# Kernel optimization log

Hardware: AMD Instinct MI355X
Metric: run time of the kernel (lower is better)

Reference implementation:

```python
import jax, jax.numpy as jnp
import numpy as np

N = 100000   # nodes
E = 1600000  # edges (avg degree 16)
DIN, DH, DOUT = 128, 64, 40


def setup_inputs() -> dict:
    key = jax.random.key(0)
    ks = jax.random.split(key, 6)
    x = jax.random.normal(ks[0], (N, DIN), dtype=jnp.float32)
    edge_index = jax.random.randint(ks[1], (2, E), 0, N, dtype=jnp.int32)
    s1 = float(1.0 / np.sqrt(DIN))
    s2 = float(1.0 / np.sqrt(DH))
    W1 = jax.random.uniform(ks[2], (DIN, DH), jnp.float32, -s1, s1)
    b1 = jax.random.uniform(ks[3], (DH,), jnp.float32, -s1, s1)
    W2 = jax.random.uniform(ks[4], (DH, DOUT), jnp.float32, -s2, s2)
    b2 = jax.random.uniform(ks[5], (DOUT,), jnp.float32, -s2, s2)
    return {"x": x, "W1": W1, "b1": b1, "W2": W2, "b2": b2, "edge_index": edge_index}


def _gcn_conv(x, W, b, src, dst):
    """PyG GCNConv: add self-loops, symmetric degree normalization, scatter-add."""
    n = x.shape[0]
    h = x @ W  # [N, F_out] — transform before propagation (PyG order)
    ones = jnp.ones(src.shape[0], dtype=h.dtype)
    deg = jax.ops.segment_sum(ones, dst, num_segments=n) + 1.0  # +1 for self-loop
    dinv = jax.lax.rsqrt(deg)  # deg >= 1, no zero guard needed
    norm = dinv[src] * dinv[dst]  # [E]
    agg = jax.ops.segment_sum(h[src] * norm[:, None], dst, num_segments=n)
    agg = agg + h * (dinv * dinv)[:, None]  # self-loop messages
    return agg + b


def reference(x, W1, b1, W2, b2, edge_index):
    src, dst = edge_index[0], edge_index[1]
    h = jax.nn.relu(_gcn_conv(x, W1, b1, src, dst))
    out = _gcn_conv(h, W2, b2, src, dst)
    return jax.nn.log_softmax(out, axis=1)
```

## Files before the change

### kernel.cpp

```cpp
#include <hip/hip_runtime.h>
#include <math.h>

#define N_NODES 100000
#define N_EDGES 1600000
#define DIN 128
#define DH 64
#define DOUT 40

#define NB 256
#define BN 391
#define CAP 8192
#define BIN_BLOCKS 512
#define EPB 3125

typedef unsigned short u16;
typedef unsigned int u32;

__device__ inline float bf2f(u16 u) {
    return __uint_as_float(((u32)u) << 16);
}
__device__ inline u16 f2bf(float f) {
    u32 u = __float_as_uint(f);
    u32 r = (u + 0x7FFFu + ((u >> 16) & 1u)) >> 16;
    return (u16)r;
}
__device__ inline void acc4(uint2 v, float& a0, float& a1, float& a2, float& a3) {
    a0 += __uint_as_float(v.x << 16);
    a1 += __uint_as_float(v.x & 0xffff0000u);
    a2 += __uint_as_float(v.y << 16);
    a3 += __uint_as_float(v.y & 0xffff0000u);
}


__global__ __launch_bounds__(256) void k_bin(const int* __restrict__ src,
                                             const int* __restrict__ dst,
                                             int* __restrict__ gcur,
                                             u32* __restrict__ staged) {
    __shared__ int hist[NB];
    __shared__ int base[NB];
    __shared__ int cur[NB];
    int t = threadIdx.x;
    for (int i = t; i < NB; i += 256) { hist[i] = 0; cur[i] = 0; }
    __syncthreads();
    int e0 = blockIdx.x * EPB;
    int e1 = e0 + EPB; if (e1 > N_EDGES) e1 = N_EDGES;
    for (int e = e0 + t; e < e1; e += 256)
        atomicAdd(&hist[dst[e] / BN], 1);
    __syncthreads();
    for (int i = t; i < NB; i += 256) {
        int h = hist[i];
        base[i] = h ? atomicAdd(&gcur[i], h) : 0;
    }
    __syncthreads();
    for (int e = e0 + t; e < e1; e += 256) {
        int d = dst[e], s = src[e];
        int b = d / BN;
        int dl = d - b * BN;
        int r = base[b] + atomicAdd(&cur[b], 1);
        if (r < CAP) staged[(size_t)b * CAP + r] = (u32)s | ((u32)dl << 17);
    }
}


__global__ __launch_bounds__(256) void k_csr(const int* __restrict__ gcur,
                                             const u32* __restrict__ staged,
                                             int* __restrict__ csr,
                                             int4* __restrict__ meta,
                                             float* __restrict__ dinv) {
    __shared__ u32 sedge[CAP];
    __shared__ int lcsr[CAP];
    __shared__ int hist[BN];
    __shared__ int lrs[BN];
    __shared__ int cur[BN];
    __shared__ int sbuf[256];
    int b = blockIdx.x, t = threadIdx.x;

    int part = 0;
    for (int i = t; i < b; i += 256) {
        int c = gcur[i]; if (c > CAP) c = CAP;
        part += c;
    }
    sbuf[t] = part;
    __syncthreads();
    for (int off = 128; off; off >>= 1) {
        if (t < off) sbuf[t] += sbuf[t + off];
        __syncthreads();
    }
    int base_ = sbuf[0];
    __syncthreads();

    int cnt = gcur[b]; if (cnt > CAP) cnt = CAP;
    for (int i = t; i < BN; i += 256) hist[i] = 0;
    for (int i = t; i < cnt; i += 256) sedge[i] = staged[(size_t)b * CAP + i];
    __syncthreads();
    for (int i = t; i < cnt; i += 256) atomicAdd(&hist[sedge[i] >> 17], 1);
    __syncthreads();

    int v0 = (2 * t < BN) ? hist[2 * t] : 0;
    int v1 = (2 * t + 1 < BN) ? hist[2 * t + 1] : 0;
    int s = v0 + v1;
    sbuf[t] = s;
    __syncthreads();
    for (int off = 1; off < 256; off <<= 1) {
        int add = (t >= off) ? sbuf[t - off] : 0;
        __syncthreads();
        sbuf[t] += add;
        __syncthreads();
    }
    int excl = sbuf[t] - s;
    if (2 * t < BN)     { lrs[2 * t] = excl;      cur[2 * t] = excl; }
    if (2 * t + 1 < BN) { lrs[2 * t + 1] = excl + v0; cur[2 * t + 1] = excl + v0; }
    __syncthreads();

    for (int i = t; i < cnt; i += 256) {
        u32 p = sedge[i];
        int pos = atomicAdd(&cur[p >> 17], 1);
        lcsr[pos] = (int)(p & 0x1FFFF);
    }
    __syncthreads();

    for (int i = t; i < cnt; i += 256) csr[base_ + i] = lcsr[i];
    int n0 = b * BN;
    for (int i = t; i < BN; i += 256) {
        int n = n0 + i;
        if (n < N_NODES) {
            int dg = hist[i];
            float dv = rsqrtf((float)dg + 1.0f);
            meta[n] = make_int4(base_ + lrs[i], dg, __float_as_int(dv), 0);
            dinv[n] = dv;
        }
    }
}


__global__ __launch_bounds__(256) void k_gemm1(const float* __restrict__ x,
                                               const float* __restrict__ W1,
                                               const float* __restrict__ dinv,
                                               u16* __restrict__ h1s) {
    __shared__ float xs[64 * 132];
    __shared__ float wsh[DIN * DH];
    int t = threadIdx.x;
    int row0 = blockIdx.x * 64;

    for (int it = 0; it < 8; ++it) {
        int idx = (it * 256 + t) * 4;
        int r = idx >> 7, c = idx & 127;
        float4 v = make_float4(0.f, 0.f, 0.f, 0.f);
        if (row0 + r < N_NODES) v = *(const float4*)&x[(size_t)(row0 + r) * DIN + c];
        *(float4*)&xs[r * 132 + c] = v;
    }
    for (int it = 0; it < 8; ++it) {
        int idx = (it * 256 + t) * 4;
        *(float4*)&wsh[idx] = *(const float4*)&W1[idx];
    }
    __syncthreads();

    int tr = t & 15;
    int tc = t >> 4;
    float acc[4][4] = {};
    for (int k = 0; k < DIN; ++k) {
        float4 wv = *(const float4*)&wsh[k * DH + tr * 4];
#pragma unroll
        for (int i = 0; i < 4; ++i) {
            float xv = xs[(tc * 4 + i) * 132 + k];
            acc[i][0] += xv * wv.x;
            acc[i][1] += xv * wv.y;
            acc[i][2] += xv * wv.z;
            acc[i][3] += xv * wv.w;
        }
    }
#pragma unroll
    for (int i = 0; i < 4; ++i) {
        int row = row0 + tc * 4 + i;
        if (row < N_NODES) {
            float dv = dinv[row];
            ushort4 o;
            o.x = f2bf(acc[i][0] * dv);
            o.y = f2bf(acc[i][1] * dv);
            o.z = f2bf(acc[i][2] * dv);
            o.w = f2bf(acc[i][3] * dv);
            *(ushort4*)&h1s[(size_t)row * DH + tr * 4] = o;
        }
    }
}


__global__ __launch_bounds__(256) void k_agg1(const u16* __restrict__ h1s,
                                              const int4* __restrict__ meta,
                                              const int* __restrict__ csr,
                                              const float* __restrict__ b1,
                                              float* __restrict__ h1) {
    int node = blockIdx.x * 4 + (threadIdx.x >> 6);
    if (node >= N_NODES) return;
    node = __builtin_amdgcn_readfirstlane(node);
    int lane = threadIdx.x & 63;
    int es = lane >> 4, fp = lane & 15;
    int4 me = meta[node];
    int s0 = me.x, d = me.y;
    float dv = __int_as_float(me.z);
    const uint2* rows = (const uint2*)h1s;
    float a0 = 0.f, a1 = 0.f, a2 = 0.f, a3 = 0.f;
    if (es == 0) acc4(rows[(u32)(node * 16 + fp)], a0, a1, a2, a3);
    for (int base = 0; base < d; base += 64) {
        int nn = d - base; if (nn > 64) nn = 64;
        int myidx = (lane < nn) ? csr[s0 + base + lane] : 0;
        int j = 0;
        for (; j + 16 <= nn; j += 16) {
            int x0 = __builtin_amdgcn_ds_bpermute((j + es) * 4, myidx);
            int x1 = __builtin_amdgcn_ds_bpermute((j + 4 + es) * 4, myidx);
            int x2 = __builtin_amdgcn_ds_bpermute((j + 8 + es) * 4, myidx);
            int x3 = __builtin_amdgcn_ds_bpermute((j + 12 + es) * 4, myidx);
            uint2 v0 = rows[(u32)(x0 * 16 + fp)];
            uint2 v1 = rows[(u32)(x1 * 16 + fp)];
            uint2 v2 = rows[(u32)(x2 * 16 + fp)];
            uint2 v3 = rows[(u32)(x3 * 16 + fp)];
            acc4(v0, a0, a1, a2, a3);
            acc4(v1, a0, a1, a2, a3);
            acc4(v2, a0, a1, a2, a3);
            acc4(v3, a0, a1, a2, a3);
        }
        for (; j < nn; j += 4) {
            int x = __builtin_amdgcn_ds_bpermute((j + es) * 4, myidx);
            if (j + es < nn) acc4(rows[(u32)(x * 16 + fp)], a0, a1, a2, a3);
        }
    }
    a0 += __shfl_xor(a0, 16, 64); a1 += __shfl_xor(a1, 16, 64);
    a2 += __shfl_xor(a2, 16, 64); a3 += __shfl_xor(a3, 16, 64);
    a0 += __shfl_xor(a0, 32, 64); a1 += __shfl_xor(a1, 32, 64);
    a2 += __shfl_xor(a2, 32, 64); a3 += __shfl_xor(a3, 32, 64);
    if (es == 0) {
        float4 bv = ((const float4*)b1)[fp];
        float4 o;
        o.x = fmaxf(a0 * dv + bv.x, 0.f);
        o.y = fmaxf(a1 * dv + bv.y, 0.f);
        o.z = fmaxf(a2 * dv + bv.z, 0.f);
        o.w = fmaxf(a3 * dv + bv.w, 0.f);
        ((float4*)h1)[(u32)(node * 16 + fp)] = o;
    }
}


__global__ __launch_bounds__(256) void k_gemm2(const float* __restrict__ h1,
                                               const float* __restrict__ W2,
                                               const float* __restrict__ dinv,
                                               u16* __restrict__ h2s) {
    __shared__ float xs[64 * 68];
    __shared__ float wsh[DH * DOUT];
    int t = threadIdx.x;
    int row0 = blockIdx.x * 64;

    for (int it = 0; it < 4; ++it) {
        int idx = (it * 256 + t) * 4;
        int r = idx >> 6, c = idx & 63;
        float4 v = make_float4(0.f, 0.f, 0.f, 0.f);
        if (row0 + r < N_NODES) v = *(const float4*)&h1[(size_t)(row0 + r) * DH + c];
        *(float4*)&xs[r * 68 + c] = v;
    }
    for (int idx = t * 4; idx < DH * DOUT; idx += 1024) {
        *(float4*)&wsh[idx] = *(const float4*)&W2[idx];
    }
    __syncthreads();

    int fg = t & 7;
    int rg = t >> 3;
    float acc[2][5] = {};
    for (int k = 0; k < DH; ++k) {
        float x0 = xs[(rg * 2 + 0) * 68 + k];
        float x1 = xs[(rg * 2 + 1) * 68 + k];
#pragma unroll
        for (int j = 0; j < 5; ++j) {
            float w = wsh[k * DOUT + fg * 5 + j];
            acc[0][j] += x0 * w;
            acc[1][j] += x1 * w;
        }
    }
#pragma unroll
    for (int i = 0; i < 2; ++i) {
        int row = row0 + rg * 2 + i;
        if (row < N_NODES) {
            float dvv = dinv[row];
#pragma unroll
            for (int j = 0; j < 5; ++j)
                h2s[(size_t)row * 64 + fg * 5 + j] = f2bf(acc[i][j] * dvv);
        }
    }
}


__global__ __launch_bounds__(256) void k_agg2(const u16* __restrict__ h2s,
                                              const int4* __restrict__ meta,
                                              const int* __restrict__ csr,
                                              const float* __restrict__ b2,
                                              float* __restrict__ out) {
    int node = blockIdx.x * 4 + (threadIdx.x >> 6);
    if (node >= N_NODES) return;
    node = __builtin_amdgcn_readfirstlane(node);
    int lane = threadIdx.x & 63;
    int es = lane >> 4, fp = lane & 15;
    bool act = fp < 10;
    int4 me = meta[node];
    int s0 = me.x, d = me.y;
    float dv = __int_as_float(me.z);
    const uint2* rows = (const uint2*)h2s;
    float a0 = 0.f, a1 = 0.f, a2 = 0.f, a3 = 0.f;
    if (es == 0 && act) acc4(rows[(u32)(node * 16 + fp)], a0, a1, a2, a3);
    for (int base = 0; base < d; base += 64) {
        int nn = d - base; if (nn > 64) nn = 64;
        int myidx = (lane < nn) ? csr[s0 + base + lane] : 0;
        int j = 0;
        for (; j + 16 <= nn; j += 16) {
            int x0 = __builtin_amdgcn_ds_bpermute((j + es) * 4, myidx);
            int x1 = __builtin_amdgcn_ds_bpermute((j + 4 + es) * 4, myidx);
            int x2 = __builtin_amdgcn_ds_bpermute((j + 8 + es) * 4, myidx);
            int x3 = __builtin_amdgcn_ds_bpermute((j + 12 + es) * 4, myidx);
            if (act) {
                uint2 v0 = rows[(u32)(x0 * 16 + fp)];
                uint2 v1 = rows[(u32)(x1 * 16 + fp)];
                uint2 v2 = rows[(u32)(x2 * 16 + fp)];
                uint2 v3 = rows[(u32)(x3 * 16 + fp)];
                acc4(v0, a0, a1, a2, a3);
                acc4(v1, a0, a1, a2, a3);
                acc4(v2, a0, a1, a2, a3);
                acc4(v3, a0, a1, a2, a3);
            }
        }
        for (; j < nn; j += 4) {
            int x = __builtin_amdgcn_ds_bpermute((j + es) * 4, myidx);
            if (act && j + es < nn) acc4(rows[(u32)(x * 16 + fp)], a0, a1, a2, a3);
        }
    }
    a0 += __shfl_xor(a0, 16, 64); a1 += __shfl_xor(a1, 16, 64);
    a2 += __shfl_xor(a2, 16, 64); a3 += __shfl_xor(a3, 16, 64);
    a0 += __shfl_xor(a0, 32, 64); a1 += __shfl_xor(a1, 32, 64);
    a2 += __shfl_xor(a2, 32, 64); a3 += __shfl_xor(a3, 32, 64);

    float4 bv = act ? ((const float4*)b2)[fp] : make_float4(0.f, 0.f, 0.f, 0.f);
    float v0 = act ? a0 * dv + bv.x : -INFINITY;
    float v1 = act ? a1 * dv + bv.y : -INFINITY;
    float v2 = act ? a2 * dv + bv.z : -INFINITY;
    float v3 = act ? a3 * dv + bv.w : -INFINITY;
    float m = fmaxf(fmaxf(v0, v1), fmaxf(v2, v3));
    m = fmaxf(m, __shfl_xor(m, 1, 64));
    m = fmaxf(m, __shfl_xor(m, 2, 64));
    m = fmaxf(m, __shfl_xor(m, 4, 64));
    m = fmaxf(m, __shfl_xor(m, 8, 64));
    float ex = act ? (expf(v0 - m) + expf(v1 - m) + expf(v2 - m) + expf(v3 - m)) : 0.f;
    ex += __shfl_xor(ex, 1, 64);
    ex += __shfl_xor(ex, 2, 64);
    ex += __shfl_xor(ex, 4, 64);
    ex += __shfl_xor(ex, 8, 64);
    float lse = m + logf(ex);
    if (es == 0 && act) {
        float4 o = make_float4(v0 - lse, v1 - lse, v2 - lse, v3 - lse);
        *(float4*)&out[(u32)(node * 40 + fp * 4)] = o;
    }
}


extern "C" void kernel_launch(void* const* d_in, const int* in_sizes, int n_in,
                              void* d_out, int out_size, void* d_ws, size_t ws_size,
                              hipStream_t stream) {
    const float* x  = (const float*)d_in[0];
    const float* W1 = (const float*)d_in[1];
    const float* b1 = (const float*)d_in[2];
    const float* W2 = (const float*)d_in[3];
    const float* b2 = (const float*)d_in[4];
    const int* eidx = (const int*)d_in[5];
    const int* srcp = eidx;
    const int* dstp = eidx + N_EDGES;
    float* out = (float*)d_out;

    char* w = (char*)d_ws;
    int* gcur    = (int*)w;   w += sizeof(int) * NB;
    float* dinv  = (float*)w; w += sizeof(float) * N_NODES + 48;
    int4* meta   = (int4*)w;  w += sizeof(int4) * N_NODES;
    u32* staged  = (u32*)w;   w += sizeof(u32) * (size_t)NB * CAP;
    int* csr     = (int*)w;   w += sizeof(int) * N_EDGES;
    u16* h1s     = (u16*)w;   w += sizeof(u16) * (size_t)N_NODES * DH;
    float* h1    = (float*)w; w += sizeof(float) * (size_t)N_NODES * DH;
    u16* h2s     = h1s;

    hipMemsetAsync(gcur, 0, sizeof(int) * NB, stream);
    k_bin<<<BIN_BLOCKS, 256, 0, stream>>>(srcp, dstp, gcur, staged);
    k_csr<<<NB, 256, 0, stream>>>(gcur, staged, csr, meta, dinv);
    k_gemm1<<<(N_NODES + 63) / 64, 256, 0, stream>>>(x, W1, dinv, h1s);
    k_agg1<<<(N_NODES + 3) / 4, 256, 0, stream>>>(h1s, meta, csr, b1, h1);
    k_gemm2<<<(N_NODES + 63) / 64, 256, 0, stream>>>(h1, W2, dinv, h2s);
    k_agg2<<<(N_NODES + 3) / 4, 256, 0, stream>>>(h2s, meta, csr, b2, out);
}
```

Baseline: 222.0 us.

## Store features as fp16 and accumulate aggregation with packed half2 adds

Intermediate node features move from bf16 storage with fp32 accumulation to fp16 storage with packed half2 accumulation in both aggregation kernels, cross-lane reductions included. This cuts the unpack and add instruction count per gathered row by doing two features per packed add. The first GEMM also reads four k values per LDS load, with a new row padding. The trade is lower accumulation precision and a risk of fp16 overflow or rounding error on high-degree nodes, while gather memory traffic stays the same.

```diff
diff --git a/kernel.cpp b/kernel.cpp
--- a/kernel.cpp
+++ b/kernel.cpp
@@ -1,4 +1,5 @@
 #include <hip/hip_runtime.h>
+#include <hip/hip_fp16.h>
 #include <math.h>
 
 #define N_NODES 100000
@@ -16,19 +17,11 @@
 typedef unsigned short u16;
 typedef unsigned int u32;
 
-__device__ inline float bf2f(u16 u) {
-    return __uint_as_float(((u32)u) << 16);
-}
-__device__ inline u16 f2bf(float f) {
-    u32 u = __float_as_uint(f);
-    u32 r = (u + 0x7FFFu + ((u >> 16) & 1u)) >> 16;
-    return (u16)r;
-}
-__device__ inline void acc4(uint2 v, float& a0, float& a1, float& a2, float& a3) {
-    a0 += __uint_as_float(v.x << 16);
-    a1 += __uint_as_float(v.x & 0xffff0000u);
-    a2 += __uint_as_float(v.y << 16);
-    a3 += __uint_as_float(v.y & 0xffff0000u);
+__device__ inline __half2 u2h(u32 u) {
+    union { u32 x; __half2 h; } c; c.x = u; return c.h;
+}
+__device__ inline u32 h2u(__half2 h) {
+    union { __half2 h; u32 x; } c; c.h = h; return c.x;
 }
 
 
@@ -137,7 +130,7 @@
                                                const float* __restrict__ W1,
                                                const float* __restrict__ dinv,
                                                u16* __restrict__ h1s) {
-    __shared__ float xs[64 * 132];
+    __shared__ float xs[64 * 140];
     __shared__ float wsh[DIN * DH];
     int t = threadIdx.x;
     int row0 = blockIdx.x * 64;
@@ -147,7 +140,7 @@
         int r = idx >> 7, c = idx & 127;
         float4 v = make_float4(0.f, 0.f, 0.f, 0.f);
         if (row0 + r < N_NODES) v = *(const float4*)&x[(size_t)(row0 + r) * DIN + c];
-        *(float4*)&xs[r * 132 + c] = v;
+        *(float4*)&xs[r * 140 + c] = v;
     }
     for (int it = 0; it < 8; ++it) {
         int idx = (it * 256 + t) * 4;
@@ -158,15 +151,22 @@
     int tr = t & 15;
     int tc = t >> 4;
     float acc[4][4] = {};
-    for (int k = 0; k < DIN; ++k) {
-        float4 wv = *(const float4*)&wsh[k * DH + tr * 4];
+    for (int kb = 0; kb < DIN; kb += 4) {
+        float4 w0 = *(const float4*)&wsh[(kb + 0) * DH + tr * 4];
+        float4 w1 = *(const float4*)&wsh[(kb + 1) * DH + tr * 4];
+        float4 w2 = *(const float4*)&wsh[(kb + 2) * DH + tr * 4];
+        float4 w3 = *(const float4*)&wsh[(kb + 3) * DH + tr * 4];
 #pragma unroll
         for (int i = 0; i < 4; ++i) {
-            float xv = xs[(tc * 4 + i) * 132 + k];
-            acc[i][0] += xv * wv.x;
-            acc[i][1] += xv * wv.y;
-            acc[i][2] += xv * wv.z;
-            acc[i][3] += xv * wv.w;
+            float4 xv = *(const float4*)&xs[(tc * 4 + i) * 140 + kb];
+            acc[i][0] += xv.x * w0.x; acc[i][1] += xv.x * w0.y;
+            acc[i][2] += xv.x * w0.z; acc[i][3] += xv.x * w0.w;
+            acc[i][0] += xv.y * w1.x; acc[i][1] += xv.y * w1.y;
+            acc[i][2] += xv.y * w1.z; acc[i][3] += xv.y * w1.w;
+            acc[i][0] += xv.z * w2.x; acc[i][1] += xv.z * w2.y;
+            acc[i][2] += xv.z * w2.z; acc[i][3] += xv.z * w2.w;
+            acc[i][0] += xv.w * w3.x; acc[i][1] += xv.w * w3.y;
+            acc[i][2] += xv.w * w3.z; acc[i][3] += xv.w * w3.w;
         }
     }
 #pragma unroll
@@ -175,10 +175,10 @@
         if (row < N_NODES) {
             float dv = dinv[row];
             ushort4 o;
-            o.x = f2bf(acc[i][0] * dv);
-            o.y = f2bf(acc[i][1] * dv);
-            o.z = f2bf(acc[i][2] * dv);
-            o.w = f2bf(acc[i][3] * dv);
+            o.x = __half_as_ushort(__float2half(acc[i][0] * dv));
+            o.y = __half_as_ushort(__float2half(acc[i][1] * dv));
+            o.z = __half_as_ushort(__float2half(acc[i][2] * dv));
+            o.w = __half_as_ushort(__float2half(acc[i][3] * dv));
             *(ushort4*)&h1s[(size_t)row * DH + tr * 4] = o;
         }
     }
@@ -199,8 +199,11 @@
     int s0 = me.x, d = me.y;
     float dv = __int_as_float(me.z);
     const uint2* rows = (const uint2*)h1s;
-    float a0 = 0.f, a1 = 0.f, a2 = 0.f, a3 = 0.f;
-    if (es == 0) acc4(rows[(u32)(node * 16 + fp)], a0, a1, a2, a3);
+    __half2 A01 = __float2half2_rn(0.f), A23 = __float2half2_rn(0.f);
+    if (es == 0) {
+        uint2 v = rows[(u32)(node * 16 + fp)];
+        A01 = u2h(v.x); A23 = u2h(v.y);
+    }
     for (int base = 0; base < d; base += 64) {
         int nn = d - base; if (nn > 64) nn = 64;
         int myidx = (lane < nn) ? csr[s0 + base + lane] : 0;
@@ -214,27 +217,30 @@
             uint2 v1 = rows[(u32)(x1 * 16 + fp)];
             uint2 v2 = rows[(u32)(x2 * 16 + fp)];
             uint2 v3 = rows[(u32)(x3 * 16 + fp)];
-            acc4(v0, a0, a1, a2, a3);
-            acc4(v1, a0, a1, a2, a3);
-            acc4(v2, a0, a1, a2, a3);
-            acc4(v3, a0, a1, a2, a3);
+            A01 = __hadd2(A01, u2h(v0.x)); A23 = __hadd2(A23, u2h(v0.y));
+            A01 = __hadd2(A01, u2h(v1.x)); A23 = __hadd2(A23, u2h(v1.y));
+            A01 = __hadd2(A01, u2h(v2.x)); A23 = __hadd2(A23, u2h(v2.y));
+            A01 = __hadd2(A01, u2h(v3.x)); A23 = __hadd2(A23, u2h(v3.y));
         }
         for (; j < nn; j += 4) {
             int x = __builtin_amdgcn_ds_bpermute((j + es) * 4, myidx);
-            if (j + es < nn) acc4(rows[(u32)(x * 16 + fp)], a0, a1, a2, a3);
-        }
-    }
-    a0 += __shfl_xor(a0, 16, 64); a1 += __shfl_xor(a1, 16, 64);
-    a2 += __shfl_xor(a2, 16, 64); a3 += __shfl_xor(a3, 16, 64);
-    a0 += __shfl_xor(a0, 32, 64); a1 += __shfl_xor(a1, 32, 64);
-    a2 += __shfl_xor(a2, 32, 64); a3 += __shfl_xor(a3, 32, 64);
+            if (j + es < nn) {
+                uint2 v = rows[(u32)(x * 16 + fp)];
+                A01 = __hadd2(A01, u2h(v.x)); A23 = __hadd2(A23, u2h(v.y));
+            }
+        }
+    }
+    A01 = __hadd2(A01, u2h((u32)__shfl_xor((int)h2u(A01), 16, 64)));
+    A23 = __hadd2(A23, u2h((u32)__shfl_xor((int)h2u(A23), 16, 64)));
+    A01 = __hadd2(A01, u2h((u32)__shfl_xor((int)h2u(A01), 32, 64)));
+    A23 = __hadd2(A23, u2h((u32)__shfl_xor((int)h2u(A23), 32, 64)));
     if (es == 0) {
         float4 bv = ((const float4*)b1)[fp];
         float4 o;
-        o.x = fmaxf(a0 * dv + bv.x, 0.f);
-        o.y = fmaxf(a1 * dv + bv.y, 0.f);
-        o.z = fmaxf(a2 * dv + bv.z, 0.f);
-        o.w = fmaxf(a3 * dv + bv.w, 0.f);
+        o.x = fmaxf(__low2float(A01)  * dv + bv.x, 0.f);
+        o.y = fmaxf(__high2float(A01) * dv + bv.y, 0.f);
+        o.z = fmaxf(__low2float(A23)  * dv + bv.z, 0.f);
+        o.w = fmaxf(__high2float(A23) * dv + bv.w, 0.f);
         ((float4*)h1)[(u32)(node * 16 + fp)] = o;
     }
 }
@@ -281,7 +287,8 @@
             float dvv = dinv[row];
 #pragma unroll
             for (int j = 0; j < 5; ++j)
-                h2s[(size_t)row * 64 + fg * 5 + j] = f2bf(acc[i][j] * dvv);
+                h2s[(size_t)row * 64 + fg * 5 + j] =
+                    __half_as_ushort(__float2half(acc[i][j] * dvv));
         }
     }
 }
@@ -302,8 +309,11 @@
     int s0 = me.x, d = me.y;
     float dv = __int_as_float(me.z);
     const uint2* rows = (const uint2*)h2s;
-    float a0 = 0.f, a1 = 0.f, a2 = 0.f, a3 = 0.f;
-    if (es == 0 && act) acc4(rows[(u32)(node * 16 + fp)], a0, a1, a2, a3);
+    __half2 A01 = __float2half2_rn(0.f), A23 = __float2half2_rn(0.f);
+    if (es == 0 && act) {
+        uint2 v = rows[(u32)(node * 16 + fp)];
+        A01 = u2h(v.x); A23 = u2h(v.y);
+    }
     for (int base = 0; base < d; base += 64) {
         int nn = d - base; if (nn > 64) nn = 64;
         int myidx = (lane < nn) ? csr[s0 + base + lane] : 0;
@@ -318,27 +328,30 @@
                 uint2 v1 = rows[(u32)(x1 * 16 + fp)];
                 uint2 v2 = rows[(u32)(x2 * 16 + fp)];
                 uint2 v3 = rows[(u32)(x3 * 16 + fp)];
-                acc4(v0, a0, a1, a2, a3);
-                acc4(v1, a0, a1, a2, a3);
-                acc4(v2, a0, a1, a2, a3);
-                acc4(v3, a0, a1, a2, a3);
+                A01 = __hadd2(A01, u2h(v0.x)); A23 = __hadd2(A23, u2h(v0.y));
+                A01 = __hadd2(A01, u2h(v1.x)); A23 = __hadd2(A23, u2h(v1.y));
+                A01 = __hadd2(A01, u2h(v2.x)); A23 = __hadd2(A23, u2h(v2.y));
+                A01 = __hadd2(A01, u2h(v3.x)); A23 = __hadd2(A23, u2h(v3.y));
             }
         }
         for (; j < nn; j += 4) {
             int x = __builtin_amdgcn_ds_bpermute((j + es) * 4, myidx);
-            if (act && j + es < nn) acc4(rows[(u32)(x * 16 + fp)], a0, a1, a2, a3);
-        }
-    }
-    a0 += __shfl_xor(a0, 16, 64); a1 += __shfl_xor(a1, 16, 64);
-    a2 += __shfl_xor(a2, 16, 64); a3 += __shfl_xor(a3, 16, 64);
-    a0 += __shfl_xor(a0, 32, 64); a1 += __shfl_xor(a1, 32, 64);
-    a2 += __shfl_xor(a2, 32, 64); a3 += __shfl_xor(a3, 32, 64);
+            if (act && j + es < nn) {
+                uint2 v = rows[(u32)(x * 16 + fp)];
+                A01 = __hadd2(A01, u2h(v.x)); A23 = __hadd2(A23, u2h(v.y));
+            }
+        }
+    }
+    A01 = __hadd2(A01, u2h((u32)__shfl_xor((int)h2u(A01), 16, 64)));
+    A23 = __hadd2(A23, u2h((u32)__shfl_xor((int)h2u(A23), 16, 64)));
+    A01 = __hadd2(A01, u2h((u32)__shfl_xor((int)h2u(A01), 32, 64)));
+    A23 = __hadd2(A23, u2h((u32)__shfl_xor((int)h2u(A23), 32, 64)));
 
     float4 bv = act ? ((const float4*)b2)[fp] : make_float4(0.f, 0.f, 0.f, 0.f);
-    float v0 = act ? a0 * dv + bv.x : -INFINITY;
-    float v1 = act ? a1 * dv + bv.y : -INFINITY;
-    float v2 = act ? a2 * dv + bv.z : -INFINITY;
-    float v3 = act ? a3 * dv + bv.w : -INFINITY;
+    float v0 = act ? __low2float(A01)  * dv + bv.x : -INFINITY;
+    float v1 = act ? __high2float(A01) * dv + bv.y : -INFINITY;
+    float v2 = act ? __low2float(A23)  * dv + bv.z : -INFINITY;
+    float v3 = act ? __high2float(A23) * dv + bv.w : -INFINITY;
     float m = fmaxf(fmaxf(v0, v1), fmaxf(v2, v3));
     m = fmaxf(m, __shfl_xor(m, 1, 64));
     m = fmaxf(m, __shfl_xor(m, 2, 64));
```

Result: no change. 217.9 us (-1.8%).
